# Optimization experiments

Measured on AMD Instinct MI355X. Metric: run time of the kernel, lower is better.

The kernel has to match this reference:

```python
import jax, jax.numpy as jnp
import numpy as np

N = 100000   # nodes
E = 1600000  # edges
G = 64       # graphs in batch
D = 128      # node_dim
H = 128      # hid_dim
OUT = 10     # out_dim (classes)
L = 3        # max_layer GIN layers per branch
BN_EPS = 1e-5


def setup_inputs() -> dict:
    key = jax.random.key(0)
    ks = jax.random.split(key, 24)
    p = lambda k, shape: (jax.random.normal(k, shape, jnp.float32) * 0.05)
    inp = {
        "x": jax.random.normal(ks[0], (N, D), jnp.float32),
        "edge_index": jax.random.randint(ks[1], (2, E), 0, N, jnp.int32),
        "batch": jnp.sort(jax.random.randint(ks[2], (N,), 0, G, jnp.int32)),
        # branch A: conv1 + convs  (stacked per-layer params; node_dim == hid_dim)
        "W1a": p(ks[3], (L, D, H)), "b1a": p(ks[4], (L, H)),
        "W2a": p(ks[5], (L, H, H)), "b2a": p(ks[6], (L, H)),
        "ga": jnp.ones((L, H), jnp.float32), "bta": jnp.zeros((L, H), jnp.float32),
        # branch B: conv2 + convs2
        "W1b": p(ks[7], (L, D, H)), "b1b": p(ks[8], (L, H)),
        "W2b": p(ks[9], (L, H, H)), "b2b": p(ks[10], (L, H)),
        "gb": jnp.ones((L, H), jnp.float32), "btb": jnp.zeros((L, H), jnp.float32),
        # heads
        "lin1_w": p(ks[11], (2 * H, H)), "lin1_b": p(ks[12], (H,)),
        "lin2_w": p(ks[13], (H, OUT)), "lin2_b": p(ks[14], (OUT,)),
        # bilinear discriminator (nn.Bilinear(H, H, 1))
        "disc_w": p(ks[15], (H, H)), "disc_b": jnp.zeros((), jnp.float32),
    }
    return inp


def _gin(h, src, dst, W1, b1, W2, b2, g, bt):
    # GINConv (eps=0): MLP(x + sum_{j->i} x_j); MLP = Lin-ReLU-Lin-ReLU-BN
    agg = jax.ops.segment_sum(h[src], dst, num_segments=N)  # scatter-add over edges
    h = h + agg
    h = jax.nn.relu(h @ W1 + b1)
    h = jax.nn.relu(h @ W2 + b2)
    mu = h.mean(0)
    var = jnp.mean((h - mu) ** 2, axis=0)
    return (h - mu) * jax.lax.rsqrt(var + BN_EPS) * g + bt


def reference(x, edge_index, batch, W1a, b1a, W2a, b2a, ga, bta,
              W1b, b1b, W2b, b2b, gb, btb, lin1_w, lin1_b, lin2_w, lin2_b,
              disc_w, disc_b):
    src, dst = edge_index[0], edge_index[1]
    counts = jnp.clip(jax.ops.segment_sum(jnp.ones((N,), x.dtype), batch, num_segments=G), 1.0)

    # branch A: conv1 + convs -> per-graph mean pool
    h = x
    for i in range(L):
        h = _gin(h, src, dst, W1a[i], b1a[i], W2a[i], b2a[i], ga[i], bta[i])
    mean_a = jax.ops.segment_sum(h, batch, num_segments=G) / counts[:, None]  # [G,H]

    # branch B (subgraph branch, run on the same graph): conv2 + convs2 -> pool
    hb = x
    for i in range(L):
        hb = _gin(hb, src, dst, W1b[i], b1b[i], W2b[i], b2b[i], gb[i], btb[i])
    pool_x = jax.ops.segment_sum(hb, batch, num_segments=G) / counts[:, None]  # [G,H]

    # MI discriminator: shuffle index as in Net.MI
    idx = jnp.arange(G - 1, -1, -1)
    idx = idx.at[G // 2].set(idx[G // 2 + 1])
    shuffled = pool_x[idx]
    bil = lambda a, c: jnp.einsum('gd,de,ge->g', a, disc_w, c) + disc_b
    logits = jnp.concatenate([bil(pool_x, pool_x), bil(pool_x, shuffled)])  # [2G]

    # classification head: cat(mean_pool, pool_x) -> lin1 -> relu -> lin2 -> log_softmax
    z = jnp.concatenate([mean_a, pool_x], axis=-1)
    z = jax.nn.relu(z @ lin1_w + lin1_b)
    z = z @ lin2_w + lin2_b
    predicts = jax.nn.log_softmax(z, axis=-1)  # [G,OUT]

    return jnp.concatenate([predicts.ravel(), logits.ravel()])  # [G*OUT + 2G]
```

## Files before the change

### kernel.cpp

```cpp
#include <hip/hip_runtime.h>
#include <hip/hip_bf16.h>

#define NN 100000
#define EE 1600000
#define GG 64
#define HH 128
#define LL 3
#define BN_EPS 1e-5f
#define NBUCK 196
#define BCAP 12288
#define PART_CHUNK 8192
#define NREP 16

typedef __attribute__((ext_vector_type(8))) short bf16x8;
typedef __attribute__((ext_vector_type(4))) float f32x4;
typedef unsigned int uint32;

__device__ __forceinline__ unsigned short f2bf(float f) {
    uint32 x = __float_as_uint(f);
    uint32 r = (x + 0x7fffu + ((x >> 16) & 1u)) >> 16;
    return (unsigned short)r;
}
__device__ __forceinline__ float bf2f(unsigned short u) { return __uint_as_float(((uint32)u) << 16); }
__device__ __forceinline__ void accq(float4& a, uint32 u, float sc) {
    a.x += sc * (float)(u & 0xffu);
    a.y += sc * (float)((u >> 8) & 0xffu);
    a.z += sc * (float)((u >> 16) & 0xffu);
    a.w += sc * (float)(u >> 24);
}
__device__ __forceinline__ void accqs(float4& a, uint32 u, float sc) {
    a.x += sc * (float)((int)(u << 24) >> 24);
    a.y += sc * (float)((int)(u << 16) >> 24);
    a.z += sc * (float)((int)(u << 8) >> 24);
    a.w += sc * (float)((int)u >> 24);
}

__global__ __launch_bounds__(256) void partition_kernel(
    const int* __restrict__ src, const int* __restrict__ dst,
    int* __restrict__ bcnt, uint32* __restrict__ part) {
    __shared__ int cnt[NBUCK];
    __shared__ int loff[NBUCK + 1];
    __shared__ int gpos[NBUCK];
    __shared__ int lcur[NBUCK];
    __shared__ uint32 buf[PART_CHUNK];
    int tid = threadIdx.x;
    int base = blockIdx.x * PART_CHUNK;
    int n = min(PART_CHUNK, EE - base);
    for (int i = tid; i < NBUCK; i += 256) { cnt[i] = 0; lcur[i] = 0; }
    __syncthreads();
    for (int i = tid; i < n; i += 256) atomicAdd(&cnt[dst[base + i] >> 9], 1);
    __syncthreads();
    if (tid == 0) {
        int acc = 0;
        for (int b = 0; b < NBUCK; ++b) { loff[b] = acc; acc += cnt[b]; }
        loff[NBUCK] = acc;
    }
    __syncthreads();
    if (tid < NBUCK && cnt[tid] > 0) gpos[tid] = atomicAdd(&bcnt[tid], cnt[tid]);
    __syncthreads();
    for (int i = tid; i < n; i += 256) {
        int d = dst[base + i];
        int s = src[base + i];
        int b = d >> 9;
        int slot = atomicAdd(&lcur[b], 1);
        buf[loff[b] + slot] = (uint32)s | ((uint32)(d & 511) << 17);
    }
    __syncthreads();
    for (int i = tid; i < n; i += 256) {
        int lo = 0, hi = NBUCK;
        while (hi - lo > 1) { int mid = (lo + hi) >> 1; if (loff[mid] <= i) lo = mid; else hi = mid; }
        part[(size_t)lo * BCAP + gpos[lo] + (i - loff[lo])] = buf[i];
    }
}

__global__ __launch_bounds__(256) void build_col_kernel(
    const uint32* __restrict__ part, const int* __restrict__ bcnt,
    int* __restrict__ col, int2* __restrict__ rowpair) {
    __shared__ int ldeg[512];
    __shared__ int loffn[512];
    __shared__ int lcur[512];
    __shared__ int pscan[256];
    __shared__ int cl[BCAP];
    int b = blockIdx.x;
    int tid = threadIdx.x;
    int node0 = b << 9;
    int nn = min(node0 + 512, NN) - node0;
    int cnt = bcnt[b];
    int base = b * BCAP;
    const uint32* pp = part + (size_t)base;
    for (int i = tid; i < 512; i += 256) { ldeg[i] = 0; lcur[i] = 0; }
    __syncthreads();
    for (int i = tid; i < cnt; i += 256) atomicAdd(&ldeg[pp[i] >> 17], 1);
    __syncthreads();
    int t2 = tid * 2;
    int a0 = ldeg[t2], a1 = ldeg[t2 + 1];
    int ps = a0 + a1;
    pscan[tid] = ps;
    __syncthreads();
    for (int off = 1; off < 256; off <<= 1) {
        int v = (tid >= off) ? pscan[tid - off] : 0;
        __syncthreads();
        pscan[tid] += v;
        __syncthreads();
    }
    int eo = pscan[tid] - ps;
    loffn[t2] = eo;
    loffn[t2 + 1] = eo + a0;
    if (t2 < nn)     rowpair[node0 + t2]     = make_int2(base + eo, base + eo + a0);
    if (t2 + 1 < nn) rowpair[node0 + t2 + 1] = make_int2(base + eo + a0, base + eo + a0 + a1);
    __syncthreads();
    for (int i = tid; i < cnt; i += 256) {
        uint32 v = pp[i];
        int dl = (int)(v >> 17);
        int pos = atomicAdd(&lcur[dl], 1);
        cl[loffn[dl] + pos] = (int)(v & 0x1FFFFu);
    }
    __syncthreads();
    for (int i = tid; i < cnt; i += 256) col[base + i] = cl[i];
}

__global__ void counts_kernel(const int* __restrict__ batch, float* __restrict__ cnt, int n) {
    __shared__ int h[GG];
    int tid = threadIdx.x;
    if (tid < GG) h[tid] = 0;
    __syncthreads();
    int i = blockIdx.x * 256 + tid;
    if (i < n) atomicAdd(&h[batch[i]], 1);
    __syncthreads();
    if (tid < GG && h[tid]) atomicAdd(&cnt[tid], (float)h[tid]);
}

__global__ void x_to_i8_kernel(const float* __restrict__ x, unsigned short* __restrict__ x8,
                               float* __restrict__ sc0) {
    int row = (blockIdx.x * 256 + threadIdx.x) >> 6;
    int lane = threadIdx.x & 63;
    if (row >= NN) return;
    float2 v = ((const float2*)x)[(size_t)row * 64 + lane];
    float m = fmaxf(fabsf(v.x), fabsf(v.y));
#pragma unroll
    for (int off = 1; off < 64; off <<= 1) m = fmaxf(m, __shfl_xor(m, off));
    float scale = m * (1.f / 127.f);
    float inv = (m > 0.f) ? 127.f / m : 0.f;
    int b0 = __float2int_rn(v.x * inv);
    int b1 = __float2int_rn(v.y * inv);
    unsigned short pk = (unsigned short)((b0 & 0xff) | ((b1 & 0xff) << 8));
    x8[(size_t)row * 64 + lane] = pk;
    if (lane == 0) sc0[row] = scale;
}

#define MAT_STRIDE 16384

__global__ void convert_w_kernel(const float* __restrict__ W1a, const float* __restrict__ W2a,
                                 const float* __restrict__ W1b, const float* __restrict__ W2b,
                                 unsigned short* __restrict__ out) {
    int t = blockIdx.x * 256 + threadIdx.x;
    if (t >= 24576) return;
    int lane = t & 63;
    int r = t >> 6;
    int ks = r & 3; r >>= 2;
    int nt = r & 7; r >>= 3;
    int mat = r & 1; r >>= 1;
    int l = r % 3, br = r / 3;
    const float* W = br ? (mat ? W2b : W1b) : (mat ? W2a : W1a);
    const float* Wl = W + (size_t)l * 128 * 128;
    int n0 = nt * 16 + (lane & 15);
    int k0 = ks * 32 + (lane >> 4) * 8;
    unsigned short tmp[8];
#pragma unroll
    for (int j = 0; j < 8; ++j) tmp[j] = f2bf(Wl[(size_t)(k0 + j) * 128 + n0]);
    size_t seq = (size_t)(br * 3 + l) * 2 + mat;
    size_t off = (((seq * 8 + nt) * 4 + ks) * 64 + (size_t)lane) * 8;
    *(uint4*)(out + off) = *(const uint4*)tmp;
}

__global__ void bn_coefs_kernel(const float* __restrict__ statsRep,
                                const float* __restrict__ ga, const float* __restrict__ bta,
                                const float* __restrict__ gb, const float* __restrict__ btb,
                                int l, float* __restrict__ coef) {
    int t = threadIdx.x;
    int br = t >> 7, cc = t & 127;
    const float* base = statsRep + (size_t)((l * 2 + br) * NREP) * 256;
    float s = 0.f, sq = 0.f;
#pragma unroll
    for (int rep = 0; rep < NREP; ++rep) {
        s += base[rep * 256 + cc];
        sq += base[rep * 256 + 128 + cc];
    }
    float mu = s * (1.f / NN);
    float var = sq * (1.f / NN) - mu * mu;
    float gm = (br ? gb : ga)[l * 128 + cc];
    float A = gm * rsqrtf(var + BN_EPS);
    float B = (br ? btb : bta)[l * 128 + cc] - mu * A;
    coef[br * 256 + cc] = A;
    coef[br * 256 + 128 + cc] = B;
}

__global__ void gather0_kernel(const uint32* __restrict__ x8, const float* __restrict__ sc0,
                               const int2* __restrict__ rowpair, const int* __restrict__ col,
                               uint2* __restrict__ out) {
    int gw = (blockIdx.x * blockDim.x + threadIdx.x) >> 6;
    int lane = threadIdx.x & 63;
    if (gw >= NN) return;
    int slot = lane >> 5;
    int c = lane & 31;
    float4 accA = {0.f, 0.f, 0.f, 0.f};
    float4 accB = {0.f, 0.f, 0.f, 0.f};
    if (slot == 0) accqs(accA, x8[(size_t)gw * 32 + c], sc0[gw]);
    int2 be = rowpair[gw];
    int beg = be.x, end = be.y;
    for (int base = beg; base < end; base += 64) {
        int nb = min(64, end - base);
        int colv = col[base + min(lane, nb - 1)];
        int k = 0;
        for (; k + 4 <= nb; k += 4) {
            int j0 = __shfl(colv, k + slot);
            int j1 = __shfl(colv, k + 2 + slot);
            float s0 = sc0[j0], s1 = sc0[j1];
            uint32 u0 = x8[(size_t)j0 * 32 + c];
            uint32 u1 = x8[(size_t)j1 * 32 + c];
            accqs(accA, u0, s0);
            accqs(accB, u1, s1);
        }
        for (; k + 2 <= nb; k += 2) {
            int j = __shfl(colv, k + slot);
            accqs(accA, x8[(size_t)j * 32 + c], sc0[j]);
        }
        if (k < nb) {
            int j = __shfl(colv, k);
            if (slot == 0) accqs(accA, x8[(size_t)j * 32 + c], sc0[j]);
        }
    }
    accA.x += accB.x; accA.y += accB.y; accA.z += accB.z; accA.w += accB.w;
    accA.x += __shfl_xor(accA.x, 32);
    accA.y += __shfl_xor(accA.y, 32);
    accA.z += __shfl_xor(accA.z, 32);
    accA.w += __shfl_xor(accA.w, 32);
    if (slot == 0) {
        uint2 o;
        o.x = (uint32)f2bf(accA.x) | ((uint32)f2bf(accA.y) << 16);
        o.y = (uint32)f2bf(accA.z) | ((uint32)f2bf(accA.w) << 16);
        out[(size_t)gw * 32 + c] = o;
    }
}

__global__ void gather_dual_kernel(const uint32* __restrict__ y8, const float* __restrict__ scales,
                                   const int2* __restrict__ rowpair, const int* __restrict__ col,
                                   const float* __restrict__ coef, uint2* __restrict__ out) {
    int gw = (blockIdx.x * blockDim.x + threadIdx.x) >> 6;
    int lane = threadIdx.x & 63;
    if (gw >= NN) return;
    int br = lane >> 5;
    int c32 = lane & 31;
    float4 A4 = ((const float4*)(coef + br * 256))[c32];
    float4 B4 = ((const float4*)(coef + br * 256 + 128))[c32];
    float4 accA = {0.f, 0.f, 0.f, 0.f};
    float4 accB = {0.f, 0.f, 0.f, 0.f};
    {
        uint32 us = y8[(size_t)gw * 64 + lane];
        accq(accA, us, scales[gw * 2 + br]);
    }
    int2 be = rowpair[gw];
    int beg = be.x, end = be.y;
    float degp1 = (float)(end - beg + 1);
    const float2* sc2 = (const float2*)scales;
    for (int base = beg; base < end; base += 64) {
        int nb = min(64, end - base);
        int colv = col[base + min(lane, nb - 1)];
        int k = 0;
        for (; k + 4 <= nb; k += 4) {
            int j0 = __builtin_amdgcn_readlane(colv, k);
            int j1 = __builtin_amdgcn_readlane(colv, k + 1);
            int j2 = __builtin_amdgcn_readlane(colv, k + 2);
            int j3 = __builtin_amdgcn_readlane(colv, k + 3);
            float2 s0 = sc2[j0];
            float2 s1 = sc2[j1];
            float2 s2 = sc2[j2];
            float2 s3 = sc2[j3];
            uint32 u0 = y8[(size_t)j0 * 64 + lane];
            uint32 u1 = y8[(size_t)j1 * 64 + lane];
            uint32 u2 = y8[(size_t)j2 * 64 + lane];
            uint32 u3 = y8[(size_t)j3 * 64 + lane];
            accq(accA, u0, br ? s0.y : s0.x);
            accq(accB, u1, br ? s1.y : s1.x);
            accq(accA, u2, br ? s2.y : s2.x);
            accq(accB, u3, br ? s3.y : s3.x);
        }
        for (; k < nb; ++k) {
            int j = __builtin_amdgcn_readlane(colv, k);
            float2 s = sc2[j];
            accq(accA, y8[(size_t)j * 64 + lane], br ? s.y : s.x);
        }
    }
    float o0 = A4.x * (accA.x + accB.x) + B4.x * degp1;
    float o1 = A4.y * (accA.y + accB.y) + B4.y * degp1;
    float o2 = A4.z * (accA.z + accB.z) + B4.z * degp1;
    float o3 = A4.w * (accA.w + accB.w) + B4.w * degp1;
    uint2 o;
    o.x = (uint32)f2bf(o0) | ((uint32)f2bf(o1) << 16);
    o.y = (uint32)f2bf(o2) | ((uint32)f2bf(o3) << 16);
    out[(size_t)gw * 64 + lane] = o;
}

#define LDS_W1 16384
#define LDS_HS (8 * 16 * 136)
__global__ __launch_bounds__(512, 4) void mlp_dual_kernel(
    const unsigned short* __restrict__ X, int in_stride, int in_off_mul,
    const unsigned short* __restrict__ wf_all,
    const float* __restrict__ b1a, const float* __restrict__ b1b,
    const float* __restrict__ b2a, const float* __restrict__ b2b,
    int l, int quant,
    unsigned short* __restrict__ Y, unsigned char* __restrict__ Y8,
    float* __restrict__ scales, float* __restrict__ statsRep, int n) {
    extern __shared__ unsigned short lds_all[];
    unsigned short* w1s = lds_all;
    unsigned short (*hs)[16][136] = (unsigned short (*)[16][136])(lds_all + LDS_W1);
    float* ssum = (float*)(lds_all + LDS_W1 + LDS_HS);
    float* ssq = ssum + 128;

    int br = blockIdx.y;
    const unsigned short* Wf = wf_all + (size_t)(br * 3 + l) * 2 * MAT_STRIDE;
    const float* b1 = (br ? b1b : b1a) + l * 128;
    const float* b2 = (br ? b2b : b2a) + l * 128;
    float* statsp = statsRep + (size_t)((l * 2 + br) * NREP + (blockIdx.x & (NREP - 1))) * 256;
    int in_off = in_off_mul * br;

    int tid = threadIdx.x;
    int wv = tid >> 6, lane = tid & 63;
    int quad = lane >> 4, l16 = lane & 15;

    const bf16x8* w2g = (const bf16x8*)(Wf + MAT_STRIDE);

    bf16x8 w2p[2][4];
#pragma unroll
    for (int p = 0; p < 2; ++p)
#pragma unroll
        for (int ks = 0; ks < 4; ++ks) w2p[p][ks] = w2g[(p * 4 + ks) * 64 + lane];

    int row0 = blockIdx.x * 128 + wv * 16;

    bf16x8 aF[4];
    {
        int r = row0 + l16;
        if (r >= n) r = n - 1;
        const unsigned short* xrow = X + (size_t)r * in_stride + in_off;
#pragma unroll
        for (int ks = 0; ks < 4; ++ks) aF[ks] = *(const bf16x8*)(xrow + ks * 32 + quad * 8);
    }

    {
        const uint4* srcp = (const uint4*)Wf;
        uint4* dstp = (uint4*)w1s;
        for (int i = tid; i < 2048; i += 512) dstp[i] = srcp[i];
    }
    if (tid < 128) { ssum[tid] = 0.f; ssq[tid] = 0.f; }
    __syncthreads();

    f32x4 acc1[8];
#pragma unroll
    for (int nt = 0; nt < 8; ++nt) {
        f32x4 c = {0.f, 0.f, 0.f, 0.f};
#pragma unroll
        for (int ks = 0; ks < 4; ++ks) {
            bf16x8 bfrag = *(const bf16x8*)(&w1s[((nt * 4 + ks) * 64 + lane) * 8]);
            c = __builtin_amdgcn_mfma_f32_16x16x32_bf16(aF[ks], bfrag, c, 0, 0, 0);
        }
        acc1[nt] = c;
    }

#pragma unroll
    for (int nt = 0; nt < 8; ++nt) {
        int c0 = nt * 16 + l16;
        float bb = b1[c0];
#pragma unroll
        for (int r = 0; r < 4; ++r) {
            float v = fmaxf(acc1[nt][r] + bb, 0.f);
            hs[wv][quad * 4 + r][c0] = f2bf(v);
        }
    }

    bf16x8 aH[4];
#pragma unroll
    for (int ks = 0; ks < 4; ++ks)
        aH[ks] = *(const bf16x8*)(&hs[wv][l16][ks * 32 + quad * 8]);

    f32x4 acc2_[8];
#pragma unroll
    for (int nt = 0; nt < 8; ++nt) {
        bf16x8 bf0, bf1, bf2, bf3;
        if (nt < 2) { bf0 = w2p[nt][0]; bf1 = w2p[nt][1]; bf2 = w2p[nt][2]; bf3 = w2p[nt][3]; }
        else {
            bf0 = w2g[(nt * 4 + 0) * 64 + lane];
            bf1 = w2g[(nt * 4 + 1) * 64 + lane];
            bf2 = w2g[(nt * 4 + 2) * 64 + lane];
            bf3 = w2g[(nt * 4 + 3) * 64 + lane];
        }
        f32x4 c = {0.f, 0.f, 0.f, 0.f};
        c = __builtin_amdgcn_mfma_f32_16x16x32_bf16(aH[0], bf0, c, 0, 0, 0);
        c = __builtin_amdgcn_mfma_f32_16x16x32_bf16(aH[1], bf1, c, 0, 0, 0);
        c = __builtin_amdgcn_mfma_f32_16x16x32_bf16(aH[2], bf2, c, 0, 0, 0);
        c = __builtin_amdgcn_mfma_f32_16x16x32_bf16(aH[3], bf3, c, 0, 0, 0);
        acc2_[nt] = c;
    }

#pragma unroll
    for (int nt = 0; nt < 8; ++nt) {
        int c0 = nt * 16 + l16;
        float bb = b2[c0];
        float s = 0.f, sq = 0.f;
#pragma unroll
        for (int r = 0; r < 4; ++r) {
            float v = fmaxf(acc2_[nt][r] + bb, 0.f);
            if (row0 + quad * 4 + r >= n) v = 0.f;
            acc2_[nt][r] = v;
            s += v; sq += v * v;
        }
        s += __shfl_xor(s, 16); s += __shfl_xor(s, 32);
        sq += __shfl_xor(sq, 16); sq += __shfl_xor(sq, 32);
        if (quad == 0) { atomicAdd(&ssum[c0], s); atomicAdd(&ssq[c0], sq); }
    }

    unsigned char* hs8 = (unsigned char*)&hs[wv][0][0];
    if (!quant) {
#pragma unroll
        for (int nt = 0; nt < 8; ++nt) {
            int c0 = nt * 16 + l16;
#pragma unroll
            for (int r = 0; r < 4; ++r) hs[wv][quad * 4 + r][c0] = f2bf(acc2_[nt][r]);
        }
        int grow = row0 + l16;
        if (grow < n) {
#pragma unroll
            for (int j = 0; j < 4; ++j) {
                uint4 v = *(const uint4*)(&hs[wv][l16][quad * 32 + j * 8]);
                *(uint4*)(Y + (size_t)grow * 256 + br * 128 + quad * 32 + j * 8) = v;
            }
        }
    } else {
#pragma unroll
        for (int r = 0; r < 4; ++r) {
            float m = acc2_[0][r];
#pragma unroll
            for (int nt = 1; nt < 8; ++nt) m = fmaxf(m, acc2_[nt][r]);
            m = fmaxf(m, __shfl_xor(m, 1));
            m = fmaxf(m, __shfl_xor(m, 2));
            m = fmaxf(m, __shfl_xor(m, 4));
            m = fmaxf(m, __shfl_xor(m, 8));
            float sc = m * (1.f / 255.f);
            float inv = (m > 0.f) ? 255.f / m : 0.f;
            int grow = row0 + quad * 4 + r;
            if (l16 == r && grow < n) scales[grow * 2 + br] = sc;
#pragma unroll
            for (int nt = 0; nt < 8; ++nt) {
                uint32 u = (uint32)__float2int_rn(acc2_[nt][r] * inv);
                hs8[(quad * 4 + r) * 144 + nt * 16 + l16] = (unsigned char)u;
            }
        }
        int grow = row0 + l16;
        if (grow < n) {
            *(uint4*)(Y8 + (size_t)grow * 256 + br * 128 + quad * 32) =
                *(const uint4*)(hs8 + l16 * 144 + quad * 32);
            *(uint4*)(Y8 + (size_t)grow * 256 + br * 128 + quad * 32 + 16) =
                *(const uint4*)(hs8 + l16 * 144 + quad * 32 + 16);
        }
    }
    __syncthreads();
    if (tid < 128) {
        atomicAdd(&statsp[tid], ssum[tid]);
        atomicAdd(&statsp[128 + tid], ssq[tid]);
    }
}

#define POOL_CHUNK 128
__global__ void pool_dual_kernel(const unsigned short* __restrict__ h,
                                 const float* __restrict__ coef2,
                                 const int* __restrict__ batch,
                                 float* __restrict__ poolA, float* __restrict__ poolB, int n) {
    int t = threadIdx.x;
    int br = t >> 7, cc = t & 127;
    float a = coef2[br * 256 + cc];
    float b = coef2[br * 256 + 128 + cc];
    float* pool = br ? poolB : poolA;

    int i0 = blockIdx.x * POOL_CHUNK;
    if (i0 >= n) return;
    int i1 = min(i0 + POOL_CHUNK, n);
    float acc = 0.f;
    int cur = batch[i0];
    for (int i = i0; i < i1; ++i) {
        int g = batch[i];
        if (g != cur) {
            atomicAdd(&pool[cur * 128 + cc], acc);
            acc = 0.f;
            cur = g;
        }
        acc += a * bf2f(h[(size_t)i * 256 + t]) + b;
    }
    atomicAdd(&pool[cur * 128 + cc], acc);
}

__global__ void disc_kernel(const float* __restrict__ poolB, const float* __restrict__ cnt,
                            const float* __restrict__ W, const float* __restrict__ db,
                            float* __restrict__ out) {
    int g = blockIdx.x, e = threadIdx.x;
    __shared__ float rs[128], rh[128];
    float invc = 1.f / fmaxf(cnt[g], 1.f);
    int gs = (g == 32) ? 30 : (63 - g);
    float invcs = 1.f / fmaxf(cnt[gs], 1.f);
    const float* a = poolB + g * 128;
    float t = 0.f;
    for (int d = 0; d < 128; ++d) t += a[d] * W[d * 128 + e];
    t *= invc;
    rs[e] = t * poolB[g * 128 + e] * invc;
    rh[e] = t * poolB[gs * 128 + e] * invcs;
    __syncthreads();
    for (int s = 64; s > 0; s >>= 1) {
        if (e < s) { rs[e] += rs[e + s]; rh[e] += rh[e + s]; }
        __syncthreads();
    }
    if (e == 0) {
        out[GG * 10 + g] = rs[0] + db[0];
        out[GG * 10 + GG + g] = rh[0] + db[0];
    }
}

__global__ void head_kernel(const float* __restrict__ poolA, const float* __restrict__ poolB,
                            const float* __restrict__ cnt,
                            const float* __restrict__ w1, const float* __restrict__ b1,
                            const float* __restrict__ w2, const float* __restrict__ b2,
                            float* __restrict__ out) {
    int g = blockIdx.x, j = threadIdx.x;
    __shared__ float s1[128];
    __shared__ float s2[10];
    __shared__ float lse;
    float invc = 1.f / fmaxf(cnt[g], 1.f);
    const float* ma = poolA + g * 128;
    const float* px = poolB + g * 128;
    float acc = b1[j];
    for (int k = 0; k < 128; ++k) acc += ma[k] * invc * w1[k * 128 + j];
    for (int k = 0; k < 128; ++k) acc += px[k] * invc * w1[(128 + k) * 128 + j];
    s1[j] = fmaxf(acc, 0.f);
    __syncthreads();
    if (j < 10) {
        float a = b2[j];
        for (int k = 0; k < 128; ++k) a += s1[k] * w2[k * 10 + j];
        s2[j] = a;
    }
    __syncthreads();
    if (j == 0) {
        float m = s2[0];
        for (int o = 1; o < 10; ++o) m = fmaxf(m, s2[o]);
        float se = 0.f;
        for (int o = 0; o < 10; ++o) se += expf(s2[o] - m);
        lse = m + logf(se);
    }
    __syncthreads();
    if (j < 10) out[g * 10 + j] = s2[j] - lse;
}

extern "C" void kernel_launch(void* const* d_in, const int* in_sizes, int n_in,
                              void* d_out, int out_size, void* d_ws, size_t ws_size,
                              hipStream_t stream) {
    const float* x     = (const float*)d_in[0];
    const int*   ei    = (const int*)d_in[1];
    const int*   batch = (const int*)d_in[2];
    const float* W1a = (const float*)d_in[3];
    const float* b1a = (const float*)d_in[4];
    const float* W2a = (const float*)d_in[5];
    const float* b2a = (const float*)d_in[6];
    const float* ga  = (const float*)d_in[7];
    const float* bta = (const float*)d_in[8];
    const float* W1b = (const float*)d_in[9];
    const float* b1b = (const float*)d_in[10];
    const float* W2b = (const float*)d_in[11];
    const float* b2b = (const float*)d_in[12];
    const float* gb  = (const float*)d_in[13];
    const float* btb = (const float*)d_in[14];
    const float* lin1_w = (const float*)d_in[15];
    const float* lin1_b = (const float*)d_in[16];
    const float* lin2_w = (const float*)d_in[17];
    const float* lin2_b = (const float*)d_in[18];
    const float* disc_w = (const float*)d_in[19];
    const float* disc_b = (const float*)d_in[20];
    float* out = (float*)d_out;

    const int* src = ei;
    const int* dst = ei + EE;

    size_t o = 0;
    auto take = [&](size_t b) { size_t p = o; o = (o + b + 255) & ~(size_t)255; return p; };
    uint8_t* w = (uint8_t*)d_ws;
    size_t o_x8   = take((size_t)NN * 128);
    size_t o_sc0  = take((size_t)NN * 4);
    size_t o_g0   = take((size_t)NN * 128 * 2);
    size_t o_bufP = take((size_t)NN * 256 * 2);
    size_t o_gbuf = take((size_t)NN * 256 * 2);
    size_t o_y8a  = take((size_t)NN * 256);
    size_t o_y8b  = take((size_t)NN * 256);
    size_t o_scA  = take((size_t)NN * 2 * 4);
    size_t o_scB  = take((size_t)NN * 2 * 4);
    size_t o_wf   = take((size_t)12 * MAT_STRIDE * 2);
    size_t o_col  = take((size_t)NBUCK * BCAP * 4);
    size_t o_part = take((size_t)NBUCK * BCAP * 4);
    size_t o_rowpair = take((size_t)NN * 8);
    size_t o_coef = take((size_t)3 * 2 * 256 * 4);
    size_t zero_begin = o;
    size_t o_bcnt   = take((size_t)NBUCK * 4);
    size_t o_stats  = take((size_t)6 * NREP * 256 * 4);
    size_t o_cnt    = take(GG * 4);
    size_t o_poolA  = take((size_t)GG * 128 * 4);
    size_t o_poolB  = take((size_t)GG * 128 * 4);
    size_t zero_end = o;

    unsigned short* x8 = (unsigned short*)(w + o_x8);
    float* sc0 = (float*)(w + o_sc0);
    uint32* g0 = (uint32*)(w + o_g0);
    unsigned short* bufP = (unsigned short*)(w + o_bufP);
    unsigned short* gbuf = (unsigned short*)(w + o_gbuf);
    unsigned char* y8a = (unsigned char*)(w + o_y8a);
    unsigned char* y8b = (unsigned char*)(w + o_y8b);
    float* scA = (float*)(w + o_scA);
    float* scB = (float*)(w + o_scB);
    unsigned short* wf = (unsigned short*)(w + o_wf);
    int* col = (int*)(w + o_col);
    uint32* part = (uint32*)(w + o_part);
    int2* rowpair = (int2*)(w + o_rowpair);
    float* coef = (float*)(w + o_coef);
    int* bcnt = (int*)(w + o_bcnt);
    float* statsRep = (float*)(w + o_stats);
    float* cnt = (float*)(w + o_cnt);
    float* poolA = (float*)(w + o_poolA);
    float* poolB = (float*)(w + o_poolB);

    hipMemsetAsync(w + zero_begin, 0, zero_end - zero_begin, stream);

    x_to_i8_kernel<<<(NN * 64 + 255) / 256, 256, 0, stream>>>(x, x8, sc0);
    convert_w_kernel<<<(24576 + 255) / 256, 256, 0, stream>>>(W1a, W2a, W1b, W2b, wf);

    partition_kernel<<<(EE + PART_CHUNK - 1) / PART_CHUNK, 256, 0, stream>>>(src, dst, bcnt, part);
    build_col_kernel<<<NBUCK, 256, 0, stream>>>(part, bcnt, col, rowpair);
    counts_kernel<<<(NN + 255) / 256, 256, 0, stream>>>(batch, cnt, NN);

    int gatherBlocks = (NN + 3) / 4;
    dim3 mlpGrid((NN + 127) / 128, 2);
    size_t ldsBytes = (size_t)LDS_W1 * 2 + (size_t)LDS_HS * 2 + 256 * 4;

    gather0_kernel<<<gatherBlocks, 256, 0, stream>>>((const uint32*)x8, sc0, rowpair, col, (uint2*)g0);

    mlp_dual_kernel<<<mlpGrid, 512, ldsBytes, stream>>>(
        (const unsigned short*)g0, 128, 0, wf, b1a, b1b, b2a, b2b, 0, 1,
        nullptr, y8a, scA, statsRep, NN);
    bn_coefs_kernel<<<1, 256, 0, stream>>>(statsRep, ga, bta, gb, btb, 0, coef + 0 * 512);

    gather_dual_kernel<<<gatherBlocks, 256, 0, stream>>>(
        (const uint32*)y8a, scA, rowpair, col, coef + 0 * 512, (uint2*)gbuf);
    mlp_dual_kernel<<<mlpGrid, 512, ldsBytes, stream>>>(
        gbuf, 256, 128, wf, b1a, b1b, b2a, b2b, 1, 1,
        nullptr, y8b, scB, statsRep, NN);
    bn_coefs_kernel<<<1, 256, 0, stream>>>(statsRep, ga, bta, gb, btb, 1, coef + 1 * 512);

    gather_dual_kernel<<<gatherBlocks, 256, 0, stream>>>(
        (const uint32*)y8b, scB, rowpair, col, coef + 1 * 512, (uint2*)gbuf);
    mlp_dual_kernel<<<mlpGrid, 512, ldsBytes, stream>>>(
        gbuf, 256, 128, wf, b1a, b1b, b2a, b2b, 2, 0,
        bufP, nullptr, nullptr, statsRep, NN);
    bn_coefs_kernel<<<1, 256, 0, stream>>>(statsRep, ga, bta, gb, btb, 2, coef + 2 * 512);

    pool_dual_kernel<<<(NN + POOL_CHUNK - 1) / POOL_CHUNK, 256, 0, stream>>>(
        bufP, coef + 2 * 512, batch, poolA, poolB, NN);
    disc_kernel<<<GG, 128, 0, stream>>>(poolB, cnt, disc_w, disc_b, out);
    head_kernel<<<GG, 128, 0, stream>>>(poolA, poolB, cnt, lin1_w, lin1_b, lin2_w, lin2_b, out);
}
```

Before: 658.8 us.

## Fuse edge gather into GIN MLP kernel and drop intermediate bf16 buffers

Replaces the separate gather kernels and the MLP kernel with one kernel. Each wave aggregates its 16 nodes' neighbor int8 features straight into LDS, then runs the two MFMA layers from there, so the bf16 aggregation buffers are never written to or read back from global memory. Layer 0 now stores x as offset-binary uint8 and applies a 128*sum(scale) correction, and runs both branches over one shared gather. W1 is read from global instead of being staged in LDS. Blocks are smaller (64 rows, 256 threads), and in layers 1 and 2 each branch's grid gathers only its own half of y8, so per-edge loads are narrower.

```diff
diff --git a/kernel.cpp b/kernel.cpp
--- a/kernel.cpp
+++ b/kernel.cpp
@@ -22,18 +22,6 @@
     return (unsigned short)r;
 }
 __device__ __forceinline__ float bf2f(unsigned short u) { return __uint_as_float(((uint32)u) << 16); }
-__device__ __forceinline__ void accq(float4& a, uint32 u, float sc) {
-    a.x += sc * (float)(u & 0xffu);
-    a.y += sc * (float)((u >> 8) & 0xffu);
-    a.z += sc * (float)((u >> 16) & 0xffu);
-    a.w += sc * (float)(u >> 24);
-}
-__device__ __forceinline__ void accqs(float4& a, uint32 u, float sc) {
-    a.x += sc * (float)((int)(u << 24) >> 24);
-    a.y += sc * (float)((int)(u << 16) >> 24);
-    a.z += sc * (float)((int)(u << 8) >> 24);
-    a.w += sc * (float)((int)u >> 24);
-}
 
 __global__ __launch_bounds__(256) void partition_kernel(
     const int* __restrict__ src, const int* __restrict__ dst,
@@ -141,8 +129,8 @@
     for (int off = 1; off < 64; off <<= 1) m = fmaxf(m, __shfl_xor(m, off));
     float scale = m * (1.f / 127.f);
     float inv = (m > 0.f) ? 127.f / m : 0.f;
-    int b0 = __float2int_rn(v.x * inv);
-    int b1 = __float2int_rn(v.y * inv);
+    int b0 = __float2int_rn(v.x * inv) + 128;
+    int b1 = __float2int_rn(v.y * inv) + 128;
     unsigned short pk = (unsigned short)((b0 & 0xff) | ((b1 & 0xff) << 8));
     x8[(size_t)row * 64 + lane] = pk;
     if (lane == 0) sc0[row] = scale;
@@ -195,278 +183,228 @@
     coef[br * 256 + 128 + cc] = B;
 }
 
-__global__ void gather0_kernel(const uint32* __restrict__ x8, const float* __restrict__ sc0,
-                               const int2* __restrict__ rowpair, const int* __restrict__ col,
-                               uint2* __restrict__ out) {
-    int gw = (blockIdx.x * blockDim.x + threadIdx.x) >> 6;
-    int lane = threadIdx.x & 63;
-    if (gw >= NN) return;
-    int slot = lane >> 5;
-    int c = lane & 31;
-    float4 accA = {0.f, 0.f, 0.f, 0.f};
-    float4 accB = {0.f, 0.f, 0.f, 0.f};
-    if (slot == 0) accqs(accA, x8[(size_t)gw * 32 + c], sc0[gw]);
-    int2 be = rowpair[gw];
-    int beg = be.x, end = be.y;
-    for (int base = beg; base < end; base += 64) {
-        int nb = min(64, end - base);
-        int colv = col[base + min(lane, nb - 1)];
-        int k = 0;
-        for (; k + 4 <= nb; k += 4) {
-            int j0 = __shfl(colv, k + slot);
-            int j1 = __shfl(colv, k + 2 + slot);
-            float s0 = sc0[j0], s1 = sc0[j1];
-            uint32 u0 = x8[(size_t)j0 * 32 + c];
-            uint32 u1 = x8[(size_t)j1 * 32 + c];
-            accqs(accA, u0, s0);
-            accqs(accB, u1, s1);
-        }
-        for (; k + 2 <= nb; k += 2) {
-            int j = __shfl(colv, k + slot);
-            accqs(accA, x8[(size_t)j * 32 + c], sc0[j]);
-        }
-        if (k < nb) {
-            int j = __shfl(colv, k);
-            if (slot == 0) accqs(accA, x8[(size_t)j * 32 + c], sc0[j]);
-        }
-    }
-    accA.x += accB.x; accA.y += accB.y; accA.z += accB.z; accA.w += accB.w;
-    accA.x += __shfl_xor(accA.x, 32);
-    accA.y += __shfl_xor(accA.y, 32);
-    accA.z += __shfl_xor(accA.z, 32);
-    accA.w += __shfl_xor(accA.w, 32);
-    if (slot == 0) {
-        uint2 o;
-        o.x = (uint32)f2bf(accA.x) | ((uint32)f2bf(accA.y) << 16);
-        o.y = (uint32)f2bf(accA.z) | ((uint32)f2bf(accA.w) << 16);
-        out[(size_t)gw * 32 + c] = o;
-    }
-}
-
-__global__ void gather_dual_kernel(const uint32* __restrict__ y8, const float* __restrict__ scales,
-                                   const int2* __restrict__ rowpair, const int* __restrict__ col,
-                                   const float* __restrict__ coef, uint2* __restrict__ out) {
-    int gw = (blockIdx.x * blockDim.x + threadIdx.x) >> 6;
-    int lane = threadIdx.x & 63;
-    if (gw >= NN) return;
-    int br = lane >> 5;
-    int c32 = lane & 31;
-    float4 A4 = ((const float4*)(coef + br * 256))[c32];
-    float4 B4 = ((const float4*)(coef + br * 256 + 128))[c32];
-    float4 accA = {0.f, 0.f, 0.f, 0.f};
-    float4 accB = {0.f, 0.f, 0.f, 0.f};
-    {
-        uint32 us = y8[(size_t)gw * 64 + lane];
-        accq(accA, us, scales[gw * 2 + br]);
-    }
-    int2 be = rowpair[gw];
-    int beg = be.x, end = be.y;
-    float degp1 = (float)(end - beg + 1);
-    const float2* sc2 = (const float2*)scales;
-    for (int base = beg; base < end; base += 64) {
-        int nb = min(64, end - base);
-        int colv = col[base + min(lane, nb - 1)];
-        int k = 0;
-        for (; k + 4 <= nb; k += 4) {
-            int j0 = __builtin_amdgcn_readlane(colv, k);
-            int j1 = __builtin_amdgcn_readlane(colv, k + 1);
-            int j2 = __builtin_amdgcn_readlane(colv, k + 2);
-            int j3 = __builtin_amdgcn_readlane(colv, k + 3);
-            float2 s0 = sc2[j0];
-            float2 s1 = sc2[j1];
-            float2 s2 = sc2[j2];
-            float2 s3 = sc2[j3];
-            uint32 u0 = y8[(size_t)j0 * 64 + lane];
-            uint32 u1 = y8[(size_t)j1 * 64 + lane];
-            uint32 u2 = y8[(size_t)j2 * 64 + lane];
-            uint32 u3 = y8[(size_t)j3 * 64 + lane];
-            accq(accA, u0, br ? s0.y : s0.x);
-            accq(accB, u1, br ? s1.y : s1.x);
-            accq(accA, u2, br ? s2.y : s2.x);
-            accq(accB, u3, br ? s3.y : s3.x);
-        }
-        for (; k < nb; ++k) {
-            int j = __builtin_amdgcn_readlane(colv, k);
-            float2 s = sc2[j];
-            accq(accA, y8[(size_t)j * 64 + lane], br ? s.y : s.x);
-        }
-    }
-    float o0 = A4.x * (accA.x + accB.x) + B4.x * degp1;
-    float o1 = A4.y * (accA.y + accB.y) + B4.y * degp1;
-    float o2 = A4.z * (accA.z + accB.z) + B4.z * degp1;
-    float o3 = A4.w * (accA.w + accB.w) + B4.w * degp1;
-    uint2 o;
-    o.x = (uint32)f2bf(o0) | ((uint32)f2bf(o1) << 16);
-    o.y = (uint32)f2bf(o2) | ((uint32)f2bf(o3) << 16);
-    out[(size_t)gw * 64 + lane] = o;
-}
-
-#define LDS_W1 16384
-#define LDS_HS (8 * 16 * 136)
-__global__ __launch_bounds__(512, 4) void mlp_dual_kernel(
-    const unsigned short* __restrict__ X, int in_stride, int in_off_mul,
+#define HS_USHORTS (4 * 16 * 136)
+__global__ __launch_bounds__(256, 4) void mlpg_kernel(
+    const unsigned char* __restrict__ Xin, int xstr, int xoffmul,
+    const float* __restrict__ sin_, int sstr, int soffmul,
+    const float* __restrict__ coefIn,
+    const int2* __restrict__ rowpair, const int* __restrict__ col,
     const unsigned short* __restrict__ wf_all,
     const float* __restrict__ b1a, const float* __restrict__ b1b,
     const float* __restrict__ b2a, const float* __restrict__ b2b,
-    int l, int quant,
+    int l, int quant, int nbr,
     unsigned short* __restrict__ Y, unsigned char* __restrict__ Y8,
     float* __restrict__ scales, float* __restrict__ statsRep, int n) {
     extern __shared__ unsigned short lds_all[];
-    unsigned short* w1s = lds_all;
-    unsigned short (*hs)[16][136] = (unsigned short (*)[16][136])(lds_all + LDS_W1);
-    float* ssum = (float*)(lds_all + LDS_W1 + LDS_HS);
-    float* ssq = ssum + 128;
-
-    int br = blockIdx.y;
-    const unsigned short* Wf = wf_all + (size_t)(br * 3 + l) * 2 * MAT_STRIDE;
-    const float* b1 = (br ? b1b : b1a) + l * 128;
-    const float* b2 = (br ? b2b : b2a) + l * 128;
-    float* statsp = statsRep + (size_t)((l * 2 + br) * NREP + (blockIdx.x & (NREP - 1))) * 256;
-    int in_off = in_off_mul * br;
-
+    unsigned short (*hs)[16][136] = (unsigned short (*)[16][136])lds_all;
+    float* ssum = (float*)(lds_all + HS_USHORTS);
+    float* ssq = ssum + 256;
+
+    int br0 = blockIdx.y;
     int tid = threadIdx.x;
     int wv = tid >> 6, lane = tid & 63;
     int quad = lane >> 4, l16 = lane & 15;
 
-    const bf16x8* w2g = (const bf16x8*)(Wf + MAT_STRIDE);
-
-    bf16x8 w2p[2][4];
-#pragma unroll
-    for (int p = 0; p < 2; ++p)
-#pragma unroll
-        for (int ks = 0; ks < 4; ++ks) w2p[p][ks] = w2g[(p * 4 + ks) * 64 + lane];
-
-    int row0 = blockIdx.x * 128 + wv * 16;
+    ssum[tid] = 0.f;
+    ssq[tid] = 0.f;
+    __syncthreads();
+
+    const unsigned char* xb = Xin + (uint32)(xoffmul * br0);
+    int ln2 = lane * 2;
+    int soff = soffmul * br0;
+    bool cf = (coefIn != nullptr);
+    float A0 = 1.f, A1 = 1.f, B0 = 0.f, B1 = 0.f;
+    if (cf) {
+        float2 a = ((const float2*)(coefIn + br0 * 256))[lane];
+        float2 b = ((const float2*)(coefIn + br0 * 256 + 128))[lane];
+        A0 = a.x; A1 = a.y; B0 = b.x; B1 = b.y;
+    }
+    int row0 = blockIdx.x * 64 + wv * 16;
+
+    for (int r = 0; r < 16; ++r) {
+        int node = row0 + r;
+        if (node >= n) node = n - 1;
+        node = __builtin_amdgcn_readfirstlane(node);
+        int2 be = rowpair[node];
+        int beg = be.x, end = be.y;
+
+        float c0a, c1a, c0b = 0.f, c1b = 0.f, S;
+        {
+            float s = sin_[(uint32)node * sstr + soff];
+            uint32 u = *(const unsigned short*)(xb + (uint32)(node * xstr) + ln2);
+            c0a = s * (float)(u & 0xffu);
+            c1a = s * (float)(u >> 8);
+            S = s;
+        }
+        for (int base = beg; base < end; base += 64) {
+            int nb = min(64, end - base);
+            int colv = col[base + min(lane, nb - 1)];
+            int k = 0;
+            for (; k + 4 <= nb; k += 4) {
+                int j0 = __builtin_amdgcn_readlane(colv, k);
+                int j1 = __builtin_amdgcn_readlane(colv, k + 1);
+                int j2 = __builtin_amdgcn_readlane(colv, k + 2);
+                int j3 = __builtin_amdgcn_readlane(colv, k + 3);
+                float s0 = sin_[(uint32)j0 * sstr + soff];
+                float s1 = sin_[(uint32)j1 * sstr + soff];
+                float s2 = sin_[(uint32)j2 * sstr + soff];
+                float s3 = sin_[(uint32)j3 * sstr + soff];
+                uint32 u0 = *(const unsigned short*)(xb + (uint32)(j0 * xstr) + ln2);
+                uint32 u1 = *(const unsigned short*)(xb + (uint32)(j1 * xstr) + ln2);
+                uint32 u2 = *(const unsigned short*)(xb + (uint32)(j2 * xstr) + ln2);
+                uint32 u3 = *(const unsigned short*)(xb + (uint32)(j3 * xstr) + ln2);
+                c0a += s0 * (float)(u0 & 0xffu); c1a += s0 * (float)(u0 >> 8);
+                c0b += s1 * (float)(u1 & 0xffu); c1b += s1 * (float)(u1 >> 8);
+                c0a += s2 * (float)(u2 & 0xffu); c1a += s2 * (float)(u2 >> 8);
+                c0b += s3 * (float)(u3 & 0xffu); c1b += s3 * (float)(u3 >> 8);
+                if (!cf) S += (s0 + s1) + (s2 + s3);
+            }
+            for (; k < nb; ++k) {
+                int j = __builtin_amdgcn_readlane(colv, k);
+                float s = sin_[(uint32)j * sstr + soff];
+                uint32 u = *(const unsigned short*)(xb + (uint32)(j * xstr) + ln2);
+                c0a += s * (float)(u & 0xffu);
+                c1a += s * (float)(u >> 8);
+                if (!cf) S += s;
+            }
+        }
+        float ch0 = c0a + c0b;
+        float ch1 = c1a + c1b;
+        float v0, v1;
+        if (cf) {
+            float dp1 = (float)(end - beg + 1);
+            v0 = A0 * ch0 + B0 * dp1;
+            v1 = A1 * ch1 + B1 * dp1;
+        } else {
+            v0 = ch0 - 128.f * S;
+            v1 = ch1 - 128.f * S;
+        }
+        uint32 o = (uint32)f2bf(v0) | ((uint32)f2bf(v1) << 16);
+        *(uint32*)(&hs[wv][r][ln2]) = o;
+    }
 
     bf16x8 aF[4];
-    {
-        int r = row0 + l16;
-        if (r >= n) r = n - 1;
-        const unsigned short* xrow = X + (size_t)r * in_stride + in_off;
-#pragma unroll
-        for (int ks = 0; ks < 4; ++ks) aF[ks] = *(const bf16x8*)(xrow + ks * 32 + quad * 8);
-    }
-
-    {
-        const uint4* srcp = (const uint4*)Wf;
-        uint4* dstp = (uint4*)w1s;
-        for (int i = tid; i < 2048; i += 512) dstp[i] = srcp[i];
-    }
-    if (tid < 128) { ssum[tid] = 0.f; ssq[tid] = 0.f; }
-    __syncthreads();
-
-    f32x4 acc1[8];
-#pragma unroll
-    for (int nt = 0; nt < 8; ++nt) {
-        f32x4 c = {0.f, 0.f, 0.f, 0.f};
-#pragma unroll
-        for (int ks = 0; ks < 4; ++ks) {
-            bf16x8 bfrag = *(const bf16x8*)(&w1s[((nt * 4 + ks) * 64 + lane) * 8]);
-            c = __builtin_amdgcn_mfma_f32_16x16x32_bf16(aF[ks], bfrag, c, 0, 0, 0);
-        }
-        acc1[nt] = c;
-    }
-
-#pragma unroll
-    for (int nt = 0; nt < 8; ++nt) {
-        int c0 = nt * 16 + l16;
-        float bb = b1[c0];
-#pragma unroll
-        for (int r = 0; r < 4; ++r) {
-            float v = fmaxf(acc1[nt][r] + bb, 0.f);
-            hs[wv][quad * 4 + r][c0] = f2bf(v);
-        }
-    }
-
-    bf16x8 aH[4];
 #pragma unroll
     for (int ks = 0; ks < 4; ++ks)
-        aH[ks] = *(const bf16x8*)(&hs[wv][l16][ks * 32 + quad * 8]);
-
-    f32x4 acc2_[8];
-#pragma unroll
-    for (int nt = 0; nt < 8; ++nt) {
-        bf16x8 bf0, bf1, bf2, bf3;
-        if (nt < 2) { bf0 = w2p[nt][0]; bf1 = w2p[nt][1]; bf2 = w2p[nt][2]; bf3 = w2p[nt][3]; }
-        else {
-            bf0 = w2g[(nt * 4 + 0) * 64 + lane];
-            bf1 = w2g[(nt * 4 + 1) * 64 + lane];
-            bf2 = w2g[(nt * 4 + 2) * 64 + lane];
-            bf3 = w2g[(nt * 4 + 3) * 64 + lane];
-        }
-        f32x4 c = {0.f, 0.f, 0.f, 0.f};
-        c = __builtin_amdgcn_mfma_f32_16x16x32_bf16(aH[0], bf0, c, 0, 0, 0);
-        c = __builtin_amdgcn_mfma_f32_16x16x32_bf16(aH[1], bf1, c, 0, 0, 0);
-        c = __builtin_amdgcn_mfma_f32_16x16x32_bf16(aH[2], bf2, c, 0, 0, 0);
-        c = __builtin_amdgcn_mfma_f32_16x16x32_bf16(aH[3], bf3, c, 0, 0, 0);
-        acc2_[nt] = c;
-    }
-
-#pragma unroll
-    for (int nt = 0; nt < 8; ++nt) {
-        int c0 = nt * 16 + l16;
-        float bb = b2[c0];
-        float s = 0.f, sq = 0.f;
-#pragma unroll
-        for (int r = 0; r < 4; ++r) {
-            float v = fmaxf(acc2_[nt][r] + bb, 0.f);
-            if (row0 + quad * 4 + r >= n) v = 0.f;
-            acc2_[nt][r] = v;
-            s += v; sq += v * v;
-        }
-        s += __shfl_xor(s, 16); s += __shfl_xor(s, 32);
-        sq += __shfl_xor(sq, 16); sq += __shfl_xor(sq, 32);
-        if (quad == 0) { atomicAdd(&ssum[c0], s); atomicAdd(&ssq[c0], sq); }
-    }
-
-    unsigned char* hs8 = (unsigned char*)&hs[wv][0][0];
-    if (!quant) {
+        aF[ks] = *(const bf16x8*)(&hs[wv][l16][ks * 32 + quad * 8]);
+
+    for (int bi = 0; bi < nbr; ++bi) {
+        int br = br0 + bi;
+        const unsigned short* Wf = wf_all + (size_t)(br * 3 + l) * 2 * MAT_STRIDE;
+        const bf16x8* w1g = (const bf16x8*)Wf;
+        const bf16x8* w2g = (const bf16x8*)(Wf + MAT_STRIDE);
+        const float* b1 = (br ? b1b : b1a) + l * 128;
+        const float* b2 = (br ? b2b : b2a) + l * 128;
+
+        f32x4 acc1[8];
+#pragma unroll
+        for (int nt = 0; nt < 8; ++nt) {
+            f32x4 c = {0.f, 0.f, 0.f, 0.f};
+#pragma unroll
+            for (int ks = 0; ks < 4; ++ks) {
+                bf16x8 bfrag = w1g[(nt * 4 + ks) * 64 + lane];
+                c = __builtin_amdgcn_mfma_f32_16x16x32_bf16(aF[ks], bfrag, c, 0, 0, 0);
+            }
+            acc1[nt] = c;
+        }
+
 #pragma unroll
         for (int nt = 0; nt < 8; ++nt) {
             int c0 = nt * 16 + l16;
-#pragma unroll
-            for (int r = 0; r < 4; ++r) hs[wv][quad * 4 + r][c0] = f2bf(acc2_[nt][r]);
-        }
-        int grow = row0 + l16;
-        if (grow < n) {
-#pragma unroll
-            for (int j = 0; j < 4; ++j) {
-                uint4 v = *(const uint4*)(&hs[wv][l16][quad * 32 + j * 8]);
-                *(uint4*)(Y + (size_t)grow * 256 + br * 128 + quad * 32 + j * 8) = v;
-            }
-        }
-    } else {
-#pragma unroll
-        for (int r = 0; r < 4; ++r) {
-            float m = acc2_[0][r];
-#pragma unroll
-            for (int nt = 1; nt < 8; ++nt) m = fmaxf(m, acc2_[nt][r]);
-            m = fmaxf(m, __shfl_xor(m, 1));
-            m = fmaxf(m, __shfl_xor(m, 2));
-            m = fmaxf(m, __shfl_xor(m, 4));
-            m = fmaxf(m, __shfl_xor(m, 8));
-            float sc = m * (1.f / 255.f);
-            float inv = (m > 0.f) ? 255.f / m : 0.f;
-            int grow = row0 + quad * 4 + r;
-            if (l16 == r && grow < n) scales[grow * 2 + br] = sc;
+            float bb = b1[c0];
+#pragma unroll
+            for (int r = 0; r < 4; ++r) {
+                float v = fmaxf(acc1[nt][r] + bb, 0.f);
+                hs[wv][quad * 4 + r][c0] = f2bf(v);
+            }
+        }
+
+        bf16x8 aH[4];
+#pragma unroll
+        for (int ks = 0; ks < 4; ++ks)
+            aH[ks] = *(const bf16x8*)(&hs[wv][l16][ks * 32 + quad * 8]);
+
+        f32x4 acc2_[8];
+#pragma unroll
+        for (int nt = 0; nt < 8; ++nt) {
+            f32x4 c = {0.f, 0.f, 0.f, 0.f};
+            c = __builtin_amdgcn_mfma_f32_16x16x32_bf16(aH[0], w2g[(nt * 4 + 0) * 64 + lane], c, 0, 0, 0);
+            c = __builtin_amdgcn_mfma_f32_16x16x32_bf16(aH[1], w2g[(nt * 4 + 1) * 64 + lane], c, 0, 0, 0);
+            c = __builtin_amdgcn_mfma_f32_16x16x32_bf16(aH[2], w2g[(nt * 4 + 2) * 64 + lane], c, 0, 0, 0);
+            c = __builtin_amdgcn_mfma_f32_16x16x32_bf16(aH[3], w2g[(nt * 4 + 3) * 64 + lane], c, 0, 0, 0);
+            acc2_[nt] = c;
+        }
+
+#pragma unroll
+        for (int nt = 0; nt < 8; ++nt) {
+            int c0 = nt * 16 + l16;
+            float bb = b2[c0];
+            float s = 0.f, sq = 0.f;
+#pragma unroll
+            for (int r = 0; r < 4; ++r) {
+                float v = fmaxf(acc2_[nt][r] + bb, 0.f);
+                if (row0 + quad * 4 + r >= n) v = 0.f;
+                acc2_[nt][r] = v;
+                s += v; sq += v * v;
+            }
+            s += __shfl_xor(s, 16); s += __shfl_xor(s, 32);
+            sq += __shfl_xor(sq, 16); sq += __shfl_xor(sq, 32);
+            if (quad == 0) { atomicAdd(&ssum[bi * 128 + c0], s); atomicAdd(&ssq[bi * 128 + c0], sq); }
+        }
+
+        unsigned char* hs8 = (unsigned char*)&hs[wv][0][0];
+        if (!quant) {
 #pragma unroll
             for (int nt = 0; nt < 8; ++nt) {
-                uint32 u = (uint32)__float2int_rn(acc2_[nt][r] * inv);
-                hs8[(quad * 4 + r) * 144 + nt * 16 + l16] = (unsigned char)u;
-            }
-        }
-        int grow = row0 + l16;
-        if (grow < n) {
-            *(uint4*)(Y8 + (size_t)grow * 256 + br * 128 + quad * 32) =
-                *(const uint4*)(hs8 + l16 * 144 + quad * 32);
-            *(uint4*)(Y8 + (size_t)grow * 256 + br * 128 + quad * 32 + 16) =
-                *(const uint4*)(hs8 + l16 * 144 + quad * 32 + 16);
-        }
-    }
-    __syncthreads();
-    if (tid < 128) {
-        atomicAdd(&statsp[tid], ssum[tid]);
-        atomicAdd(&statsp[128 + tid], ssq[tid]);
+                int c0 = nt * 16 + l16;
+#pragma unroll
+                for (int r = 0; r < 4; ++r) hs[wv][quad * 4 + r][c0] = f2bf(acc2_[nt][r]);
+            }
+            int grow = row0 + l16;
+            if (grow < n) {
+#pragma unroll
+                for (int j = 0; j < 4; ++j) {
+                    uint4 v = *(const uint4*)(&hs[wv][l16][quad * 32 + j * 8]);
+                    *(uint4*)(Y + (size_t)grow * 256 + br * 128 + quad * 32 + j * 8) = v;
+                }
+            }
+        } else {
+#pragma unroll
+            for (int r = 0; r < 4; ++r) {
+                float m = acc2_[0][r];
+#pragma unroll
+                for (int nt = 1; nt < 8; ++nt) m = fmaxf(m, acc2_[nt][r]);
+                m = fmaxf(m, __shfl_xor(m, 1));
+                m = fmaxf(m, __shfl_xor(m, 2));
+                m = fmaxf(m, __shfl_xor(m, 4));
+                m = fmaxf(m, __shfl_xor(m, 8));
+                float sc = m * (1.f / 255.f);
+                float inv = (m > 0.f) ? 255.f / m : 0.f;
+                int grow = row0 + quad * 4 + r;
+                if (l16 == r && grow < n) scales[grow * 2 + br] = sc;
+#pragma unroll
+                for (int nt = 0; nt < 8; ++nt) {
+                    uint32 u = (uint32)__float2int_rn(acc2_[nt][r] * inv);
+                    hs8[(quad * 4 + r) * 144 + nt * 16 + l16] = (unsigned char)u;
+                }
+            }
+            int grow = row0 + l16;
+            if (grow < n) {
+                *(uint4*)(Y8 + (size_t)grow * 256 + br * 128 + quad * 32) =
+                    *(const uint4*)(hs8 + l16 * 144 + quad * 32);
+                *(uint4*)(Y8 + (size_t)grow * 256 + br * 128 + quad * 32 + 16) =
+                    *(const uint4*)(hs8 + l16 * 144 + quad * 32 + 16);
+            }
+        }
+    }
+
+    __syncthreads();
+    for (int bi = 0; bi < nbr; ++bi) {
+        if (tid < 128) {
+            float* sp = statsRep + (size_t)((l * 2 + br0 + bi) * NREP + (blockIdx.x & (NREP - 1))) * 256;
+            atomicAdd(&sp[tid], ssum[bi * 128 + tid]);
+            atomicAdd(&sp[128 + tid], ssq[bi * 128 + tid]);
+        }
     }
 }
 
@@ -591,9 +529,7 @@
     uint8_t* w = (uint8_t*)d_ws;
     size_t o_x8   = take((size_t)NN * 128);
     size_t o_sc0  = take((size_t)NN * 4);
-    size_t o_g0   = take((size_t)NN * 128 * 2);
     size_t o_bufP = take((size_t)NN * 256 * 2);
-    size_t o_gbuf = take((size_t)NN * 256 * 2);
     size_t o_y8a  = take((size_t)NN * 256);
     size_t o_y8b  = take((size_t)NN * 256);
     size_t o_scA  = take((size_t)NN * 2 * 4);
@@ -613,9 +549,7 @@
 
     unsigned short* x8 = (unsigned short*)(w + o_x8);
     float* sc0 = (float*)(w + o_sc0);
-    uint32* g0 = (uint32*)(w + o_g0);
     unsigned short* bufP = (unsigned short*)(w + o_bufP);
-    unsigned short* gbuf = (unsigned short*)(w + o_gbuf);
     unsigned char* y8a = (unsigned char*)(w + o_y8a);
     unsigned char* y8b = (unsigned char*)(w + o_y8b);
     float* scA = (float*)(w + o_scA);
@@ -640,28 +574,24 @@
     build_col_kernel<<<NBUCK, 256, 0, stream>>>(part, bcnt, col, rowpair);
     counts_kernel<<<(NN + 255) / 256, 256, 0, stream>>>(batch, cnt, NN);
 
-    int gatherBlocks = (NN + 3) / 4;
-    dim3 mlpGrid((NN + 127) / 128, 2);
-    size_t ldsBytes = (size_t)LDS_W1 * 2 + (size_t)LDS_HS * 2 + 256 * 4;
-
-    gather0_kernel<<<gatherBlocks, 256, 0, stream>>>((const uint32*)x8, sc0, rowpair, col, (uint2*)g0);
-
-    mlp_dual_kernel<<<mlpGrid, 512, ldsBytes, stream>>>(
-        (const unsigned short*)g0, 128, 0, wf, b1a, b1b, b2a, b2b, 0, 1,
+    int gridX = (NN + 63) / 64;
+    size_t ldsBytes = (size_t)HS_USHORTS * 2 + 512 * 4;
+
+    mlpg_kernel<<<dim3(gridX, 1), 256, ldsBytes, stream>>>(
+        (const unsigned char*)x8, 128, 0, sc0, 1, 0, nullptr,
+        rowpair, col, wf, b1a, b1b, b2a, b2b, 0, 1, 2,
         nullptr, y8a, scA, statsRep, NN);
     bn_coefs_kernel<<<1, 256, 0, stream>>>(statsRep, ga, bta, gb, btb, 0, coef + 0 * 512);
 
-    gather_dual_kernel<<<gatherBlocks, 256, 0, stream>>>(
-        (const uint32*)y8a, scA, rowpair, col, coef + 0 * 512, (uint2*)gbuf);
-    mlp_dual_kernel<<<mlpGrid, 512, ldsBytes, stream>>>(
-        gbuf, 256, 128, wf, b1a, b1b, b2a, b2b, 1, 1,
+    mlpg_kernel<<<dim3(gridX, 2), 256, ldsBytes, stream>>>(
+        y8a, 256, 128, scA, 2, 1, coef + 0 * 512,
+        rowpair, col, wf, b1a, b1b, b2a, b2b, 1, 1, 1,
         nullptr, y8b, scB, statsRep, NN);
     bn_coefs_kernel<<<1, 256, 0, stream>>>(statsRep, ga, bta, gb, btb, 1, coef + 1 * 512);
 
-    gather_dual_kernel<<<gatherBlocks, 256, 0, stream>>>(
-        (const uint32*)y8b, scB, rowpair, col, coef + 1 * 512, (uint2*)gbuf);
-    mlp_dual_kernel<<<mlpGrid, 512, ldsBytes, stream>>>(
-        gbuf, 256, 128, wf, b1a, b1b, b2a, b2b, 2, 0,
+    mlpg_kernel<<<dim3(gridX, 2), 256, ldsBytes, stream>>>(
+        y8b, 256, 128, scB, 2, 1, coef + 1 * 512,
+        rowpair, col, wf, b1a, b1b, b2a, b2b, 2, 0, 1,
         bufP, nullptr, nullptr, statsRep, NN);
     bn_coefs_kernel<<<1, 256, 0, stream>>>(statsRep, ga, bta, gb, btb, 2, coef + 2 * 512);
 
```

Result: slower. 928.3 us (+40.9%).
